# Kernel optimization log

Hardware: AMD Instinct MI355X
Metric: run time of the kernel (lower is better)

Reference implementation:

```python
import jax, jax.numpy as jnp
import numpy as np

N = 100000  # nodes
E = 1600000  # edges
DIM_IN, DIM_H, DIM_OUT = 128, 64, 16


def gcn_conv(x, W, b, src, dst, n):
    """PyG GCNConv: symmetric-normalized aggregation with self-loops.
    out = D^{-1/2} (A + I) D^{-1/2} (x @ W) + b, degrees counted on dst.
    """
    h = x @ W  # [n, d_out]
    deg = jax.ops.segment_sum(jnp.ones((src.shape[0],), h.dtype), dst,
                              num_segments=n) + 1.0  # +1 for self-loop
    dinv = jax.lax.rsqrt(deg)  # [n]
    norm = dinv[src] * dinv[dst]  # [E]
    msg = h[src] * norm[:, None]  # [E, d_out] -- dominant memory traffic
    agg = jax.ops.segment_sum(msg, dst, num_segments=n)
    # self-loop contribution: norm_ii = dinv_i^2
    return agg + h * (dinv * dinv)[:, None] + b


def setup_inputs() -> dict:
    key = jax.random.key(0)
    k = jax.random.split(key, 6)
    x = jax.random.normal(k[0], (N, DIM_IN), dtype=jnp.float32)
    edge_index = jax.random.randint(k[1], (2, E), 0, N, dtype=jnp.int64)
    # Glorot-style init like torch Linear
    s1 = 1.0 / np.sqrt(DIM_IN)
    s2 = 1.0 / np.sqrt(DIM_H)
    W1 = jax.random.uniform(k[2], (DIM_IN, DIM_H), jnp.float32, -s1, s1)
    b1 = jnp.zeros((DIM_H,), jnp.float32)
    W2 = jax.random.uniform(k[3], (DIM_H, DIM_OUT), jnp.float32, -s2, s2)
    b2 = jnp.zeros((DIM_OUT,), jnp.float32)
    return {"x": x, "edge_index": edge_index, "W1": W1, "b1": b1,
            "W2": W2, "b2": b2}


def reference(x, edge_index, W1, b1, W2, b2):
    src, dst = edge_index[0], edge_index[1]
    n = x.shape[0]
    # dropout is identity in eval mode
    h = gcn_conv(x, W1, b1, src, dst, n)
    h = jax.nn.relu(h)
    h = gcn_conv(h, W2, b2, src, dst, n)
    return jax.nn.log_softmax(h, axis=1)
```

## Files before the change

kernel.cpp:

```cpp
#include <hip/hip_runtime.h>
#include <math.h>

#define DIM_IN 128
#define DIM_H 64
#define DIM_OUT 16
#define NBSHIFT 8
#define CHUNK 4096
#define PACKBLKS 256

typedef __attribute__((ext_vector_type(8))) short bf16x8;
typedef __attribute__((ext_vector_type(4))) float f32x4;
typedef __attribute__((ext_vector_type(2))) float f32x2;

__device__ __forceinline__ ushort f2bf(float f) {
  uint u = __float_as_uint(f);
  return (ushort)((u + 0x7FFF + ((u >> 16) & 1)) >> 16);
}
__device__ __forceinline__ float bf2f(ushort s) {
  return __uint_as_float(((uint)s) << 16);
}
__device__ __forceinline__ uint cvtpk(float lo, float hi) {
  uint r;
  asm("v_cvt_pk_bf16_f32 %0, %1, %2" : "=v"(r) : "v"(lo), "v"(hi));
  return r;
}
__device__ __forceinline__ uint f2fp8pk(float a, float b) {
  uint r = 0;
  asm("v_cvt_pk_fp8_f32 %0, %1, %2" : "+v"(r) : "v"(a), "v"(b));
  return r & 0xffffu;
}
__device__ __forceinline__ f32x2 fp8pk2f(uint u) {
  f32x2 r;
  asm("v_cvt_pk_f32_fp8 %0, %1" : "=v"(r) : "v"(u));
  return r;
}


__global__ __launch_bounds__(256) void k_hist1(const int* __restrict__ dst, int E,
                                               int* __restrict__ chunkhist) {
  __shared__ int lh[512];
  int t = threadIdx.x;
  int c = blockIdx.x;
  lh[t] = 0;
  lh[t + 256] = 0;
  __syncthreads();
  int e0 = c * CHUNK;
  int e1 = min(E, e0 + CHUNK);
  for (int i = e0 + t; i < e1; i += 256) atomicAdd(&lh[dst[i] >> NBSHIFT], 1);
  __syncthreads();
  chunkhist[c * 512 + t] = lh[t];
  chunkhist[c * 512 + t + 256] = lh[t + 256];
}

__global__ __launch_bounds__(512) void k_scanc(const int* __restrict__ chunkhist,
                                               int NC, int* __restrict__ cstart,
                                               int* __restrict__ gbhist) {
  __shared__ int sc[512];
  int t = threadIdx.x;
  int b = blockIdx.x;
  int v = (t < NC) ? chunkhist[t * 512 + b] : 0;
  sc[t] = v;
  __syncthreads();
  for (int off = 1; off < 512; off <<= 1) {
    int add = (t >= off) ? sc[t - off] : 0;
    __syncthreads();
    sc[t] += add;
    __syncthreads();
  }
  if (t < NC) cstart[t * 512 + b] = sc[t] - v;
  if (t == 511) gbhist[b] = sc[511];
}

__global__ __launch_bounds__(512) void k_bscan(const int* __restrict__ gbhist,
                                               int* __restrict__ bbase) {
  __shared__ int sb[512];
  int t = threadIdx.x;
  int v = gbhist[t];
  sb[t] = v;
  __syncthreads();
  for (int off = 1; off < 512; off <<= 1) {
    int add = (t >= off) ? sb[t - off] : 0;
    __syncthreads();
    sb[t] += add;
    __syncthreads();
  }
  bbase[t] = sb[t] - v;
}

__global__ __launch_bounds__(256) void k_part2(const int* __restrict__ src,
                                               const int* __restrict__ dst, int E,
                                               const int* __restrict__ cstart,
                                               const int* __restrict__ bbase,
                                               uint* __restrict__ pairs) {
  __shared__ int lcur[512];
  int t = threadIdx.x;
  int c = blockIdx.x;
  lcur[t] = cstart[c * 512 + t] + bbase[t];
  lcur[t + 256] = cstart[c * 512 + t + 256] + bbase[t + 256];
  __syncthreads();
  int e0 = c * CHUNK;
  int e1 = min(E, e0 + CHUNK);
  for (int i = e0 + t; i < e1; i += 256) {
    int d = dst[i];
    int pos = atomicAdd(&lcur[d >> NBSHIFT], 1);
    pairs[pos] = ((uint)src[i] << 8) | ((uint)d & 255u);
  }
}

__global__ __launch_bounds__(256) void k_csr(const uint* __restrict__ pairs,
                                             const int* __restrict__ gbhist,
                                             const int* __restrict__ bbase, int n,
                                             int* __restrict__ degi,
                                             float* __restrict__ dinv,
                                             int* __restrict__ rowptr,
                                             int* __restrict__ srcs) {
  __shared__ int nh[256];
  __shared__ int ncur[256];
  int t = threadIdx.x;
  int b = blockIdx.x;
  int base = bbase[b];
  int cnt = gbhist[b];
  nh[t] = 0;
  __syncthreads();
  for (int i = t; i < cnt; i += 256) atomicAdd(&nh[pairs[base + i] & 255u], 1);
  __syncthreads();
  int node = (b << NBSHIFT) + t;
  int v = nh[t];
  if (node < n) {
    degi[node] = v;
    dinv[node] = rsqrtf((float)v + 1.0f);
  }
  __syncthreads();
  for (int off = 1; off < 256; off <<= 1) {
    int add = (t >= off) ? nh[t - off] : 0;
    __syncthreads();
    nh[t] += add;
    __syncthreads();
  }
  int excl = nh[t] - v;
  if (node < n) rowptr[node] = base + excl;
  ncur[t] = base + excl;
  __syncthreads();
  for (int i = t; i < cnt; i += 256) {
    uint p = pairs[base + i];
    int pos = atomicAdd(&ncur[p & 255u], 1);
    srcs[pos] = (int)(p >> 8);
  }
}

__global__ __launch_bounds__(256, 4) void k_pack_gemm1(
    const int* __restrict__ srcs, const float* __restrict__ dinv,
    uint* __restrict__ esrc, int E, const float* __restrict__ x,
    const float* __restrict__ W, uchar* __restrict__ h, int n, int nTiles) {
  const int t = threadIdx.x;
  if (blockIdx.x < PACKBLKS) {
    const int stride = PACKBLKS * 256;
    for (int i = blockIdx.x * 256 + t; i < E; i += stride) {
      uint s = (uint)srcs[i];
      esrc[i] = ((uint)f2bf(dinv[s]) << 17) | s;
    }
    return;
  }
  const int lane = t & 63;
  const int wid = (blockIdx.x - PACKBLKS) * 4 + (t >> 6);
  const int nW = (gridDim.x - PACKBLKS) * 4;
  const int cc = lane & 15;
  const int kb = (lane >> 4) * 8;

  bf16x8 bfrag[4][4];
#pragma unroll
  for (int kc = 0; kc < 4; ++kc)
#pragma unroll
    for (int nt = 0; nt < 4; ++nt) {
      union { bf16x8 v; uint u[4]; } fb;
#pragma unroll
      for (int j = 0; j < 4; ++j) {
        float lo = W[(size_t)(kc * 32 + kb + 2 * j) * DIM_H + nt * 16 + cc];
        float hi = W[(size_t)(kc * 32 + kb + 2 * j + 1) * DIM_H + nt * 16 + cc];
        fb.u[j] = cvtpk(lo, hi);
      }
      bfrag[kc][nt] = fb.v;
    }

  for (int tile = wid; tile < nTiles; tile += nW) {
    int row0 = tile * 16;
    int ra = row0 + cc;
    if (ra > n - 1) ra = n - 1;
    const float* xp = x + (size_t)ra * DIM_IN;
    f32x4 acc[4] = {{0.f, 0.f, 0.f, 0.f},
                    {0.f, 0.f, 0.f, 0.f},
                    {0.f, 0.f, 0.f, 0.f},
                    {0.f, 0.f, 0.f, 0.f}};
#pragma unroll
    for (int kc = 0; kc < 4; ++kc) {
      float4 a0 = *(const float4*)(xp + kc * 32 + kb);
      float4 a1 = *(const float4*)(xp + kc * 32 + kb + 4);
      union { bf16x8 v; uint u[4]; } fa;
      fa.u[0] = cvtpk(a0.x, a0.y);
      fa.u[1] = cvtpk(a0.z, a0.w);
      fa.u[2] = cvtpk(a1.x, a1.y);
      fa.u[3] = cvtpk(a1.z, a1.w);
#pragma unroll
      for (int nt = 0; nt < 4; ++nt)
        acc[nt] = __builtin_amdgcn_mfma_f32_16x16x32_bf16(fa.v, bfrag[kc][nt],
                                                          acc[nt], 0, 0, 0);
    }
    int rbase = row0 + (lane >> 4) * 4;
#pragma unroll
    for (int nt = 0; nt < 4; ++nt) {
      int col = nt * 16 + cc;
      uint w01 = f2fp8pk(acc[nt][0], acc[nt][1]);
      uint w23 = f2fp8pk(acc[nt][2], acc[nt][3]);
      uchar bytes[4] = {(uchar)(w01 & 0xff), (uchar)(w01 >> 8),
                        (uchar)(w23 & 0xff), (uchar)(w23 >> 8)};
#pragma unroll
      for (int j = 0; j < 4; ++j) {
        int r = rbase + j;
        if (r < n) h[(size_t)r * DIM_H + col] = bytes[j];
      }
    }
  }
}

__global__ __launch_bounds__(256) void k_gemm2(const ushort* __restrict__ a,
                                               const float* __restrict__ W,
                                               ushort* __restrict__ h2, int n) {
  __shared__ float Ws[64][16];
  const int t = threadIdx.x;
  for (int i = t; i < 64 * 16; i += 256) Ws[i >> 4][i & 15] = W[i];
  __syncthreads();
  int r = blockIdx.x * 256 + t;
  if (r >= n) return;
  const uint4* ap = (const uint4*)(a + (size_t)r * DIM_H);
  float acc[16] = {};
#pragma unroll
  for (int k8 = 0; k8 < 8; ++k8) {
    uint4 v = ap[k8];
    uint w[4] = {v.x, v.y, v.z, v.w};
#pragma unroll
    for (int p = 0; p < 4; ++p) {
      float v0 = bf2f((ushort)(w[p] & 0xffff));
      float v1 = bf2f((ushort)(w[p] >> 16));
      int k = k8 * 8 + p * 2;
#pragma unroll
      for (int j = 0; j < 16; ++j) acc[j] = fmaf(v0, Ws[k][j], acc[j]);
#pragma unroll
      for (int j = 0; j < 16; ++j) acc[j] = fmaf(v1, Ws[k + 1][j], acc[j]);
    }
  }
  ushort4* hp = (ushort4*)(h2 + (size_t)r * DIM_OUT);
#pragma unroll
  for (int q = 0; q < 4; ++q) {
    ushort4 o;
    o.x = f2bf(acc[q * 4 + 0]);
    o.y = f2bf(acc[q * 4 + 1]);
    o.z = f2bf(acc[q * 4 + 2]);
    o.w = f2bf(acc[q * 4 + 3]);
    hp[q] = o;
  }
}


__global__ __launch_bounds__(256) void k_gather64(const uchar* __restrict__ h,
                                                  const uint* __restrict__ esrc,
                                                  const int* __restrict__ rowptr,
                                                  const int* __restrict__ deg,
                                                  const float* __restrict__ dinv,
                                                  const float* __restrict__ b,
                                                  ushort* __restrict__ out, int n) {
  int node = blockIdx.x * 4 + (threadIdx.x >> 6);
  int lane = threadIdx.x & 63;
  int g = lane >> 4;
  int q = lane & 15;
  if (node >= n) return;
  int start = rowptr[node];
  int cnt = deg[node];
  float dd = dinv[node];
  float a0 = 0.f, a1 = 0.f, a2 = 0.f, a3 = 0.f;
  for (int j0 = 0; j0 < cnt; j0 += 64) {
    int rem = cnt - j0;
    if (rem > 64) rem = 64;
    uint p_l = (lane < rem) ? esrc[start + j0 + lane] : 0u;
    int s_l = (int)(p_l & 0x1FFFFu);
    float w_l = bf2f((ushort)(p_l >> 17)) * dd;
    for (int j = 0; j < rem; j += 16) {
      int i0 = j + g, i1 = j + 4 + g, i2 = j + 8 + g, i3 = j + 12 + g;
      int s0 = __shfl(s_l, i0);
      float w0 = __shfl(w_l, i0);
      int s1 = __shfl(s_l, i1);
      float w1 = __shfl(w_l, i1);
      int s2 = __shfl(s_l, i2);
      float w2 = __shfl(w_l, i2);
      int s3 = __shfl(s_l, i3);
      float w3 = __shfl(w_l, i3);
      uint v0 = *(const uint*)(h + (size_t)s0 * DIM_H + q * 4);
      uint v1 = *(const uint*)(h + (size_t)s1 * DIM_H + q * 4);
      uint v2 = *(const uint*)(h + (size_t)s2 * DIM_H + q * 4);
      uint v3 = *(const uint*)(h + (size_t)s3 * DIM_H + q * 4);
      f32x2 l0 = fp8pk2f(v0), h0 = fp8pk2f(v0 >> 16);
      f32x2 l1 = fp8pk2f(v1), h1v = fp8pk2f(v1 >> 16);
      f32x2 l2 = fp8pk2f(v2), h2v = fp8pk2f(v2 >> 16);
      f32x2 l3 = fp8pk2f(v3), h3v = fp8pk2f(v3 >> 16);
      a0 = fmaf(l0.x, w0, a0);
      a1 = fmaf(l0.y, w0, a1);
      a2 = fmaf(h0.x, w0, a2);
      a3 = fmaf(h0.y, w0, a3);
      a0 = fmaf(l1.x, w1, a0);
      a1 = fmaf(l1.y, w1, a1);
      a2 = fmaf(h1v.x, w1, a2);
      a3 = fmaf(h1v.y, w1, a3);
      a0 = fmaf(l2.x, w2, a0);
      a1 = fmaf(l2.y, w2, a1);
      a2 = fmaf(h2v.x, w2, a2);
      a3 = fmaf(h2v.y, w2, a3);
      a0 = fmaf(l3.x, w3, a0);
      a1 = fmaf(l3.y, w3, a1);
      a2 = fmaf(h3v.x, w3, a2);
      a3 = fmaf(h3v.y, w3, a3);
    }
  }
  a0 += __shfl_xor(a0, 16); a0 += __shfl_xor(a0, 32);
  a1 += __shfl_xor(a1, 16); a1 += __shfl_xor(a1, 32);
  a2 += __shfl_xor(a2, 16); a2 += __shfl_xor(a2, 32);
  a3 += __shfl_xor(a3, 16); a3 += __shfl_xor(a3, 32);
  if (g == 0) {
    uint sv = *(const uint*)(h + (size_t)node * DIM_H + q * 4);
    f32x2 slo = fp8pk2f(sv), shi = fp8pk2f(sv >> 16);
    float s2 = dd * dd;
    a0 = fmaxf(fmaf(slo.x, s2, a0) + b[4 * q + 0], 0.f);
    a1 = fmaxf(fmaf(slo.y, s2, a1) + b[4 * q + 1], 0.f);
    a2 = fmaxf(fmaf(shi.x, s2, a2) + b[4 * q + 2], 0.f);
    a3 = fmaxf(fmaf(shi.y, s2, a3) + b[4 * q + 3], 0.f);
    uint lo = cvtpk(a0, a1);
    uint hi = cvtpk(a2, a3);
    *(uint2*)(out + (size_t)node * DIM_H + q * 4) = make_uint2(lo, hi);
  }
}

__global__ __launch_bounds__(256) void k_gather16(const ushort* __restrict__ h,
                                                  const uint* __restrict__ esrc,
                                                  const int* __restrict__ rowptr,
                                                  const int* __restrict__ deg,
                                                  const float* __restrict__ dinv,
                                                  const float* __restrict__ b,
                                                  float* __restrict__ out, int n) {
  int node = blockIdx.x * 16 + (threadIdx.x >> 4);
  int lane = threadIdx.x & 63;
  int lane16 = lane & 15;
  int gbase = lane & 48;
  int e = (lane >> 2) & 3;
  int c = lane & 3;
  if (node >= n) return;
  int start = rowptr[node];
  int cnt = deg[node];
  float dd = dinv[node];
  const int iA = gbase + e, iB = gbase + 4 + e, iC = gbase + 8 + e,
            iD = gbase + 12 + e;
  float a0 = 0.f, a1 = 0.f, a2 = 0.f, a3 = 0.f;
  for (int j0 = 0; j0 < cnt; j0 += 16) {
    int rem = cnt - j0;
    if (rem > 16) rem = 16;
    uint p_l = (lane16 < rem) ? esrc[start + j0 + lane16] : 0u;
    int s_l = (int)(p_l & 0x1FFFFu);
    float w_l = bf2f((ushort)(p_l >> 17)) * dd;
    int sA = __shfl(s_l, iA);
    float wA = __shfl(w_l, iA);
    int sB = __shfl(s_l, iB);
    float wB = __shfl(w_l, iB);
    int sC = __shfl(s_l, iC);
    float wC = __shfl(w_l, iC);
    int sD = __shfl(s_l, iD);
    float wD = __shfl(w_l, iD);
    uint2 vA = *(const uint2*)(h + (size_t)sA * DIM_OUT + c * 4);
    uint2 vB = *(const uint2*)(h + (size_t)sB * DIM_OUT + c * 4);
    uint2 vC = *(const uint2*)(h + (size_t)sC * DIM_OUT + c * 4);
    uint2 vD = *(const uint2*)(h + (size_t)sD * DIM_OUT + c * 4);
    a0 = fmaf(bf2f((ushort)(vA.x & 0xffff)), wA, a0);
    a1 = fmaf(bf2f((ushort)(vA.x >> 16)), wA, a1);
    a2 = fmaf(bf2f((ushort)(vA.y & 0xffff)), wA, a2);
    a3 = fmaf(bf2f((ushort)(vA.y >> 16)), wA, a3);
    a0 = fmaf(bf2f((ushort)(vB.x & 0xffff)), wB, a0);
    a1 = fmaf(bf2f((ushort)(vB.x >> 16)), wB, a1);
    a2 = fmaf(bf2f((ushort)(vB.y & 0xffff)), wB, a2);
    a3 = fmaf(bf2f((ushort)(vB.y >> 16)), wB, a3);
    a0 = fmaf(bf2f((ushort)(vC.x & 0xffff)), wC, a0);
    a1 = fmaf(bf2f((ushort)(vC.x >> 16)), wC, a1);
    a2 = fmaf(bf2f((ushort)(vC.y & 0xffff)), wC, a2);
    a3 = fmaf(bf2f((ushort)(vC.y >> 16)), wC, a3);
    a0 = fmaf(bf2f((ushort)(vD.x & 0xffff)), wD, a0);
    a1 = fmaf(bf2f((ushort)(vD.x >> 16)), wD, a1);
    a2 = fmaf(bf2f((ushort)(vD.y & 0xffff)), wD, a2);
    a3 = fmaf(bf2f((ushort)(vD.y >> 16)), wD, a3);
  }
  a0 += __shfl_xor(a0, 4); a0 += __shfl_xor(a0, 8);
  a1 += __shfl_xor(a1, 4); a1 += __shfl_xor(a1, 8);
  a2 += __shfl_xor(a2, 4); a2 += __shfl_xor(a2, 8);
  a3 += __shfl_xor(a3, 4); a3 += __shfl_xor(a3, 8);
  uint2 sv = *(const uint2*)(h + (size_t)node * DIM_OUT + c * 4);
  float s2 = dd * dd;
  a0 = fmaf(bf2f((ushort)(sv.x & 0xffff)), s2, a0) + b[4 * c + 0];
  a1 = fmaf(bf2f((ushort)(sv.x >> 16)), s2, a1) + b[4 * c + 1];
  a2 = fmaf(bf2f((ushort)(sv.y & 0xffff)), s2, a2) + b[4 * c + 2];
  a3 = fmaf(bf2f((ushort)(sv.y >> 16)), s2, a3) + b[4 * c + 3];
  float m = fmaxf(fmaxf(a0, a1), fmaxf(a2, a3));
  m = fmaxf(m, __shfl_xor(m, 1));
  m = fmaxf(m, __shfl_xor(m, 2));
  float ssum = expf(a0 - m) + expf(a1 - m) + expf(a2 - m) + expf(a3 - m);
  ssum += __shfl_xor(ssum, 1);
  ssum += __shfl_xor(ssum, 2);
  float l = m + logf(ssum);
  if (e == 0)
    *(float4*)(out + (size_t)node * DIM_OUT + c * 4) =
        make_float4(a0 - l, a1 - l, a2 - l, a3 - l);
}


extern "C" void kernel_launch(void* const* d_in, const int* in_sizes, int n_in,
                              void* d_out, int out_size, void* d_ws, size_t ws_size,
                              hipStream_t stream) {
  const float* x  = (const float*)d_in[0];
  const int*   ei = (const int*)d_in[1];
  const float* W1 = (const float*)d_in[2];
  const float* b1 = (const float*)d_in[3];
  const float* W2 = (const float*)d_in[4];
  const float* b2 = (const float*)d_in[5];
  float* out = (float*)d_out;

  const int n = in_sizes[0] / DIM_IN;
  const int E = in_sizes[1] / 2;
  const int* srcv = ei;
  const int* dstv = ei + E;
  const int NB = (n + 255) >> NBSHIFT;
  const int NC = (E + CHUNK - 1) / CHUNK;

  char* wsb = (char*)d_ws;
  int* degi      = (int*)wsb;   wsb += (size_t)n * 4;
  int* rowptr    = (int*)wsb;   wsb += (size_t)n * 4;
  float* dinv    = (float*)wsb; wsb += (size_t)n * 4;
  int* gbhist    = (int*)wsb;   wsb += 512 * 4;
  int* bbase     = (int*)wsb;   wsb += 512 * 4;
  int* chunkhist = (int*)wsb;   wsb += (size_t)512 * 512 * 4;
  int* cstart    = (int*)wsb;   wsb += (size_t)512 * 512 * 4;
  int* srcs      = (int*)wsb;   wsb += (size_t)E * 4;
  uint* esrc     = (uint*)wsb;  wsb += (size_t)E * 4;
  uchar* h1      = (uchar*)wsb; wsb += (size_t)n * DIM_H;
  ushort* agg1   = (ushort*)wsb; wsb += (size_t)n * DIM_H * 2;
  ushort* h2     = (ushort*)wsb; wsb += (size_t)n * DIM_OUT * 2;
  uint* pairs = (uint*)agg1;

  k_hist1<<<NC, 256, 0, stream>>>(dstv, E, chunkhist);
  k_scanc<<<512, 512, 0, stream>>>(chunkhist, NC, cstart, gbhist);
  k_bscan<<<1, 512, 0, stream>>>(gbhist, bbase);
  k_part2<<<NC, 256, 0, stream>>>(srcv, dstv, E, cstart, bbase, pairs);
  k_csr<<<NB, 256, 0, stream>>>(pairs, gbhist, bbase, n, degi, dinv, rowptr, srcs);

  k_pack_gemm1<<<PACKBLKS + 512, 256, 0, stream>>>(srcs, dinv, esrc, E, x, W1, h1,
                                                   n, (n + 15) / 16);

  k_gather64<<<(n + 3) / 4, 256, 0, stream>>>(h1, esrc, rowptr, degi, dinv, b1,
                                              agg1, n);

  k_gemm2<<<(n + 255) / 256, 256, 0, stream>>>(agg1, W2, h2, n);
  k_gather16<<<(n + 15) / 16, 256, 0, stream>>>(h2, esrc, rowptr, degi, dinv, b2,
                                                out, n);
}
```

Baseline: 130.8 us.

## Fold bucket scan into partition/CSR kernels and store layer-2 features as fp8

Removes the single-block k_bscan launch. Each k_part2 block now redundantly scans the 512 bucket totals itself, and each k_csr block computes its base offset with a shared-memory reduction. Separately, the layer-2 transformed features h2 are stored as fp8 instead of bf16, which halves the bytes gathered per edge in k_gather16. This saves one kernel launch and gather bandwidth, but adds redundant scan work in every block and loses precision in the final aggregation before log_softmax.

Measured after the change: 128.4 us. No clear change (-1.8%).

```diff
diff --git a/kernel.cpp b/kernel.cpp
--- a/kernel.cpp
+++ b/kernel.cpp
@@ -71,32 +71,30 @@
   if (t == 511) gbhist[b] = sc[511];
 }
 
-__global__ __launch_bounds__(512) void k_bscan(const int* __restrict__ gbhist,
-                                               int* __restrict__ bbase) {
-  __shared__ int sb[512];
-  int t = threadIdx.x;
-  int v = gbhist[t];
-  sb[t] = v;
-  __syncthreads();
-  for (int off = 1; off < 512; off <<= 1) {
-    int add = (t >= off) ? sb[t - off] : 0;
-    __syncthreads();
-    sb[t] += add;
-    __syncthreads();
-  }
-  bbase[t] = sb[t] - v;
-}
-
 __global__ __launch_bounds__(256) void k_part2(const int* __restrict__ src,
                                                const int* __restrict__ dst, int E,
                                                const int* __restrict__ cstart,
-                                               const int* __restrict__ bbase,
+                                               const int* __restrict__ gbhist,
                                                uint* __restrict__ pairs) {
+  __shared__ int sb[512];
   __shared__ int lcur[512];
   int t = threadIdx.x;
   int c = blockIdx.x;
-  lcur[t] = cstart[c * 512 + t] + bbase[t];
-  lcur[t + 256] = cstart[c * 512 + t + 256] + bbase[t + 256];
+  int v0 = gbhist[t], v1 = gbhist[t + 256];
+  sb[t] = v0;
+  sb[t + 256] = v1;
+  __syncthreads();
+  for (int off = 1; off < 256; off <<= 1) {
+    int a0 = (t >= off) ? sb[t - off] : 0;
+    int a1 = (t >= off) ? sb[256 + t - off] : 0;
+    __syncthreads();
+    sb[t] += a0;
+    sb[256 + t] += a1;
+    __syncthreads();
+  }
+  int tot0 = sb[255];
+  lcur[t] = cstart[c * 512 + t] + sb[t] - v0;
+  lcur[t + 256] = cstart[c * 512 + t + 256] + sb[256 + t] - v1 + tot0;
   __syncthreads();
   int e0 = c * CHUNK;
   int e1 = min(E, e0 + CHUNK);
@@ -108,17 +106,26 @@
 }
 
 __global__ __launch_bounds__(256) void k_csr(const uint* __restrict__ pairs,
-                                             const int* __restrict__ gbhist,
-                                             const int* __restrict__ bbase, int n,
+                                             const int* __restrict__ gbhist, int n,
                                              int* __restrict__ degi,
                                              float* __restrict__ dinv,
                                              int* __restrict__ rowptr,
                                              int* __restrict__ srcs) {
   __shared__ int nh[256];
   __shared__ int ncur[256];
+  __shared__ int red[256];
   int t = threadIdx.x;
   int b = blockIdx.x;
-  int base = bbase[b];
+  int p = 0;
+  if (t < b) p += gbhist[t];
+  if (t + 256 < b) p += gbhist[t + 256];
+  red[t] = p;
+  __syncthreads();
+  for (int s = 128; s > 0; s >>= 1) {
+    if (t < s) red[t] += red[t + s];
+    __syncthreads();
+  }
+  int base = red[0];
   int cnt = gbhist[b];
   nh[t] = 0;
   __syncthreads();
@@ -142,9 +149,9 @@
   ncur[t] = base + excl;
   __syncthreads();
   for (int i = t; i < cnt; i += 256) {
-    uint p = pairs[base + i];
-    int pos = atomicAdd(&ncur[p & 255u], 1);
-    srcs[pos] = (int)(p >> 8);
+    uint pr = pairs[base + i];
+    int pos = atomicAdd(&ncur[pr & 255u], 1);
+    srcs[pos] = (int)(pr >> 8);
   }
 }
 
@@ -224,7 +231,7 @@
 
 __global__ __launch_bounds__(256) void k_gemm2(const ushort* __restrict__ a,
                                                const float* __restrict__ W,
-                                               ushort* __restrict__ h2, int n) {
+                                               uchar* __restrict__ h2, int n) {
   __shared__ float Ws[64][16];
   const int t = threadIdx.x;
   for (int i = t; i < 64 * 16; i += 256) Ws[i >> 4][i & 15] = W[i];
@@ -248,16 +255,12 @@
       for (int j = 0; j < 16; ++j) acc[j] = fmaf(v1, Ws[k + 1][j], acc[j]);
     }
   }
-  ushort4* hp = (ushort4*)(h2 + (size_t)r * DIM_OUT);
-#pragma unroll
-  for (int q = 0; q < 4; ++q) {
-    ushort4 o;
-    o.x = f2bf(acc[q * 4 + 0]);
-    o.y = f2bf(acc[q * 4 + 1]);
-    o.z = f2bf(acc[q * 4 + 2]);
-    o.w = f2bf(acc[q * 4 + 3]);
-    hp[q] = o;
-  }
+  uint4 o;
+  o.x = f2fp8pk(acc[0], acc[1]) | (f2fp8pk(acc[2], acc[3]) << 16);
+  o.y = f2fp8pk(acc[4], acc[5]) | (f2fp8pk(acc[6], acc[7]) << 16);
+  o.z = f2fp8pk(acc[8], acc[9]) | (f2fp8pk(acc[10], acc[11]) << 16);
+  o.w = f2fp8pk(acc[12], acc[13]) | (f2fp8pk(acc[14], acc[15]) << 16);
+  *(uint4*)(h2 + (size_t)r * DIM_OUT) = o;
 }
 
 
@@ -337,7 +340,7 @@
   }
 }
 
-__global__ __launch_bounds__(256) void k_gather16(const ushort* __restrict__ h,
+__global__ __launch_bounds__(256) void k_gather16(const uchar* __restrict__ h,
                                                   const uint* __restrict__ esrc,
                                                   const int* __restrict__ rowptr,
                                                   const int* __restrict__ deg,
@@ -371,37 +374,42 @@
     float wC = __shfl(w_l, iC);
     int sD = __shfl(s_l, iD);
     float wD = __shfl(w_l, iD);
-    uint2 vA = *(const uint2*)(h + (size_t)sA * DIM_OUT + c * 4);
-    uint2 vB = *(const uint2*)(h + (size_t)sB * DIM_OUT + c * 4);
-    uint2 vC = *(const uint2*)(h + (size_t)sC * DIM_OUT + c * 4);
-    uint2 vD = *(const uint2*)(h + (size_t)sD * DIM_OUT + c * 4);
-    a0 = fmaf(bf2f((ushort)(vA.x & 0xffff)), wA, a0);
-    a1 = fmaf(bf2f((ushort)(vA.x >> 16)), wA, a1);
-    a2 = fmaf(bf2f((ushort)(vA.y & 0xffff)), wA, a2);
-    a3 = fmaf(bf2f((ushort)(vA.y >> 16)), wA, a3);
-    a0 = fmaf(bf2f((ushort)(vB.x & 0xffff)), wB, a0);
-    a1 = fmaf(bf2f((ushort)(vB.x >> 16)), wB, a1);
-    a2 = fmaf(bf2f((ushort)(vB.y & 0xffff)), wB, a2);
-    a3 = fmaf(bf2f((ushort)(vB.y >> 16)), wB, a3);
-    a0 = fmaf(bf2f((ushort)(vC.x & 0xffff)), wC, a0);
-    a1 = fmaf(bf2f((ushort)(vC.x >> 16)), wC, a1);
-    a2 = fmaf(bf2f((ushort)(vC.y & 0xffff)), wC, a2);
-    a3 = fmaf(bf2f((ushort)(vC.y >> 16)), wC, a3);
-    a0 = fmaf(bf2f((ushort)(vD.x & 0xffff)), wD, a0);
-    a1 = fmaf(bf2f((ushort)(vD.x >> 16)), wD, a1);
-    a2 = fmaf(bf2f((ushort)(vD.y & 0xffff)), wD, a2);
-    a3 = fmaf(bf2f((ushort)(vD.y >> 16)), wD, a3);
+    uint vA = *(const uint*)(h + (size_t)sA * DIM_OUT + c * 4);
+    uint vB = *(const uint*)(h + (size_t)sB * DIM_OUT + c * 4);
+    uint vC = *(const uint*)(h + (size_t)sC * DIM_OUT + c * 4);
+    uint vD = *(const uint*)(h + (size_t)sD * DIM_OUT + c * 4);
+    f32x2 lA = fp8pk2f(vA), hA = fp8pk2f(vA >> 16);
+    f32x2 lB = fp8pk2f(vB), hB = fp8pk2f(vB >> 16);
+    f32x2 lC = fp8pk2f(vC), hC = fp8pk2f(vC >> 16);
+    f32x2 lD = fp8pk2f(vD), hD = fp8pk2f(vD >> 16);
+    a0 = fmaf(lA.x, wA, a0);
+    a1 = fmaf(lA.y, wA, a1);
+    a2 = fmaf(hA.x, wA, a2);
+    a3 = fmaf(hA.y, wA, a3);
+    a0 = fmaf(lB.x, wB, a0);
+    a1 = fmaf(lB.y, wB, a1);
+    a2 = fmaf(hB.x, wB, a2);
+    a3 = fmaf(hB.y, wB, a3);
+    a0 = fmaf(lC.x, wC, a0);
+    a1 = fmaf(lC.y, wC, a1);
+    a2 = fmaf(hC.x, wC, a2);
+    a3 = fmaf(hC.y, wC, a3);
+    a0 = fmaf(lD.x, wD, a0);
+    a1 = fmaf(lD.y, wD, a1);
+    a2 = fmaf(hD.x, wD, a2);
+    a3 = fmaf(hD.y, wD, a3);
   }
   a0 += __shfl_xor(a0, 4); a0 += __shfl_xor(a0, 8);
   a1 += __shfl_xor(a1, 4); a1 += __shfl_xor(a1, 8);
   a2 += __shfl_xor(a2, 4); a2 += __shfl_xor(a2, 8);
   a3 += __shfl_xor(a3, 4); a3 += __shfl_xor(a3, 8);
-  uint2 sv = *(const uint2*)(h + (size_t)node * DIM_OUT + c * 4);
+  uint sv = *(const uint*)(h + (size_t)node * DIM_OUT + c * 4);
+  f32x2 slo = fp8pk2f(sv), shi = fp8pk2f(sv >> 16);
   float s2 = dd * dd;
-  a0 = fmaf(bf2f((ushort)(sv.x & 0xffff)), s2, a0) + b[4 * c + 0];
-  a1 = fmaf(bf2f((ushort)(sv.x >> 16)), s2, a1) + b[4 * c + 1];
-  a2 = fmaf(bf2f((ushort)(sv.y & 0xffff)), s2, a2) + b[4 * c + 2];
-  a3 = fmaf(bf2f((ushort)(sv.y >> 16)), s2, a3) + b[4 * c + 3];
+  a0 = fmaf(slo.x, s2, a0) + b[4 * c + 0];
+  a1 = fmaf(slo.y, s2, a1) + b[4 * c + 1];
+  a2 = fmaf(shi.x, s2, a2) + b[4 * c + 2];
+  a3 = fmaf(shi.y, s2, a3) + b[4 * c + 3];
   float m = fmaxf(fmaxf(a0, a1), fmaxf(a2, a3));
   m = fmaxf(m, __shfl_xor(m, 1));
   m = fmaxf(m, __shfl_xor(m, 2));
@@ -438,21 +446,19 @@
   int* rowptr    = (int*)wsb;   wsb += (size_t)n * 4;
   float* dinv    = (float*)wsb; wsb += (size_t)n * 4;
   int* gbhist    = (int*)wsb;   wsb += 512 * 4;
-  int* bbase     = (int*)wsb;   wsb += 512 * 4;
   int* chunkhist = (int*)wsb;   wsb += (size_t)512 * 512 * 4;
   int* cstart    = (int*)wsb;   wsb += (size_t)512 * 512 * 4;
   int* srcs      = (int*)wsb;   wsb += (size_t)E * 4;
   uint* esrc     = (uint*)wsb;  wsb += (size_t)E * 4;
   uchar* h1      = (uchar*)wsb; wsb += (size_t)n * DIM_H;
   ushort* agg1   = (ushort*)wsb; wsb += (size_t)n * DIM_H * 2;
-  ushort* h2     = (ushort*)wsb; wsb += (size_t)n * DIM_OUT * 2;
+  uchar* h2      = (uchar*)wsb; wsb += (size_t)n * DIM_OUT;
   uint* pairs = (uint*)agg1;
 
   k_hist1<<<NC, 256, 0, stream>>>(dstv, E, chunkhist);
   k_scanc<<<512, 512, 0, stream>>>(chunkhist, NC, cstart, gbhist);
-  k_bscan<<<1, 512, 0, stream>>>(gbhist, bbase);
-  k_part2<<<NC, 256, 0, stream>>>(srcv, dstv, E, cstart, bbase, pairs);
-  k_csr<<<NB, 256, 0, stream>>>(pairs, gbhist, bbase, n, degi, dinv, rowptr, srcs);
+  k_part2<<<NC, 256, 0, stream>>>(srcv, dstv, E, cstart, gbhist, pairs);
+  k_csr<<<NB, 256, 0, stream>>>(pairs, gbhist, n, degi, dinv, rowptr, srcs);
 
   k_pack_gemm1<<<PACKBLKS + 512, 256, 0, stream>>>(srcs, dinv, esrc, E, x, W1, h1,
                                                    n, (n + 15) / 16);
```
